# Kernel optimization log

Hardware: AMD Instinct MI355X
Metric: run time of the kernel (lower is better)

## Reference

```python
import jax, jax.numpy as jnp
import numpy as np

B, N_IN, NODE, L = 4, 128, 32, 256
N_HID, N_OUT = 64, 128
D_IN = N_HID          # d_inner = expand(1) * d_model
D_STATE = 2 * N_HID   # d_state = n_hid * 2
D_CONV = 2
DT_RANK = max(1, -(-N_HID // 16))  # ceil(d_model/16) = 4


def setup_inputs() -> dict:
    key = jax.random.key(0)
    ks = jax.random.split(key, 12)
    s = lambda k, shape, scale: (jax.random.normal(k, shape, jnp.float32) * scale)
    inputs = jax.random.normal(ks[0], (B, N_IN, NODE, L), jnp.float32)
    return {
        "inputs": inputs,
        "w_in": s(ks[1], (N_HID, N_IN), 1.0 / np.sqrt(N_IN)),
        "b_in": jnp.zeros((N_HID,), jnp.float32),
        "in_proj_w": s(ks[2], (2 * D_IN, N_HID), 1.0 / np.sqrt(N_HID)),
        "conv_w": s(ks[3], (D_IN, D_CONV), 0.5),
        "conv_b": jnp.zeros((D_IN,), jnp.float32),
        "x_proj_w": s(ks[4], (DT_RANK + 2 * D_STATE, D_IN), 1.0 / np.sqrt(D_IN)),
        "dt_proj_w": s(ks[5], (D_IN, DT_RANK), DT_RANK ** -0.5),
        "dt_proj_b": s(ks[6], (D_IN,), 0.1),
        "A_log": jnp.log(jnp.tile(jnp.arange(1, D_STATE + 1, dtype=jnp.float32)[None, :], (D_IN, 1))),
        "D": jnp.ones((D_IN,), jnp.float32),
        "out_proj_w": s(ks[7], (N_HID, D_IN), 1.0 / np.sqrt(D_IN)),
        "w_out": s(ks[8], (N_OUT, N_HID), 1.0 / np.sqrt(N_HID)),
        "b_out": jnp.zeros((N_OUT,), jnp.float32),
        "ln_w": jnp.ones((L, N_OUT), jnp.float32),
        "ln_b": jnp.zeros((L, N_OUT), jnp.float32),
    }


def _mamba(x, in_proj_w, conv_w, conv_b, x_proj_w, dt_proj_w, dt_proj_b, A_log, D, out_proj_w):
    # x: (Bseq, L, d_model)
    Bs, Ls, _ = x.shape
    d_state = A_log.shape[1]
    dt_rank = dt_proj_w.shape[1]
    d_conv = conv_w.shape[1]

    xz = x @ in_proj_w.T                     # (Bs, L, 2*d_inner)
    xm, z = jnp.split(xz, 2, axis=-1)

    # causal depthwise conv1d (padding = d_conv-1, truncated to L)
    xp = jnp.pad(xm, ((0, 0), (d_conv - 1, 0), (0, 0)))
    xc = sum(xp[:, k:k + Ls, :] * conv_w[:, k] for k in range(d_conv)) + conv_b
    xc = jax.nn.silu(xc)                     # (Bs, L, d_inner)

    dbc = xc @ x_proj_w.T                    # (Bs, L, dt_rank + 2*d_state)
    dt = dbc[..., :dt_rank]
    Bm = dbc[..., dt_rank:dt_rank + d_state]
    Cm = dbc[..., dt_rank + d_state:]
    delta = jax.nn.softplus(dt @ dt_proj_w.T + dt_proj_b)  # (Bs, L, d_inner)
    A = -jnp.exp(A_log)                      # (d_inner, d_state)

    def step(h, inp):
        dlt, Bt, Ct, xt = inp                # (Bs,d), (Bs,s), (Bs,s), (Bs,d)
        dA = jnp.exp(dlt[:, :, None] * A)    # (Bs, d, s)
        h = dA * h + (dlt * xt)[:, :, None] * Bt[:, None, :]
        y = jnp.einsum('bds,bs->bd', h, Ct)
        return h, y

    h0 = jnp.zeros((Bs, xm.shape[-1], d_state), x.dtype)
    xs = (delta.transpose(1, 0, 2), Bm.transpose(1, 0, 2),
          Cm.transpose(1, 0, 2), xc.transpose(1, 0, 2))
    _, ys = jax.lax.scan(step, h0, xs)       # ys: (L, Bs, d_inner)

    y = ys.transpose(1, 0, 2) + xc * D
    y = y * jax.nn.silu(z)
    return y @ out_proj_w.T                  # (Bs, L, d_model)


def reference(inputs, w_in, b_in, in_proj_w, conv_w, conv_b, x_proj_w,
              dt_proj_w, dt_proj_b, A_log, D, out_proj_w,
              w_out, b_out, ln_w, ln_b):
    b, n_in, node, seq = inputs.shape
    # permute(0,2,3,1).reshape(B*node, L, n_in)
    x = inputs.transpose(0, 2, 3, 1).reshape(b * node, seq, n_in)
    x = x @ w_in.T + b_in
    x = jax.nn.silu(_mamba(x, in_proj_w, conv_w, conv_b, x_proj_w,
                           dt_proj_w, dt_proj_b, A_log, D, out_proj_w))
    x = x @ w_out.T + b_out                  # (B*node, L, n_out)
    # LayerNorm over last two dims [feature_len, n_out]
    mu = x.mean(axis=(-2, -1), keepdims=True)
    var = ((x - mu) ** 2).mean(axis=(-2, -1), keepdims=True)
    x = (x - mu) / jnp.sqrt(var + 1e-5) * ln_w + ln_b
    return x.reshape(b, node, seq, -1).transpose(0, 3, 1, 2)
```

## Files before the change

### kernel.cpp

```cpp
#include <hip/hip_runtime.h>
#include <math.h>


__device__ __forceinline__ float silu_f(float v) { return v / (1.f + __expf(-v)); }
__device__ __forceinline__ float softplus_f(float v) { return v > 20.f ? v : log1pf(__expf(v)); }

__global__ __launch_bounds__(256) void k1_proj(
    const float* __restrict__ inp, const float* __restrict__ w_in,
    const float* __restrict__ b_in, const float* __restrict__ ipw,
    float* __restrict__ XM, float* __restrict__ Zb)
{
  __shared__ float sIN[128*64];
  __shared__ float sW[64*68];
  __shared__ float sXT[64*68];
  const int bid = blockIdx.x;
  const int r = bid >> 2, tb = bid & 3;
  const int b = r >> 5, node = r & 31;
  const int t0 = tb * 64;
  const int tid = threadIdx.x;
  const int tg = tid & 15, vg = tid >> 4;
  const int tl0 = tg * 4, v0 = vg * 4;

  for (int e = tid; e < 128*64; e += 256) {
    int i = e >> 6, t = e & 63;
    sIN[e] = inp[((b*128 + i)*32 + node)*256 + t0 + t];
  }

  float acc[4][4];
  #pragma unroll
  for (int ti = 0; ti < 4; ti++)
    #pragma unroll
    for (int j = 0; j < 4; j++) acc[ti][j] = b_in[v0 + j];

  for (int kc = 0; kc < 2; kc++) {
    __syncthreads();
    for (int e = tid; e < 64*16; e += 256) {
      int row = e >> 4, c4 = e & 15;
      *(float4*)&sW[row*68 + c4*4] = *(const float4*)&w_in[row*128 + kc*64 + c4*4];
    }
    __syncthreads();
    for (int k4 = 0; k4 < 16; k4++) {
      float4 wv[4];
      #pragma unroll
      for (int j = 0; j < 4; j++)
        wv[j] = *(const float4*)&sW[(v0 + j)*68 + k4*4];
      #pragma unroll
      for (int kk = 0; kk < 4; kk++) {
        float4 x4 = *(const float4*)&sIN[(kc*64 + k4*4 + kk)*64 + tl0];
        #pragma unroll
        for (int j = 0; j < 4; j++) {
          float w = kk==0 ? wv[j].x : kk==1 ? wv[j].y : kk==2 ? wv[j].z : wv[j].w;
          acc[0][j] = fmaf(x4.x, w, acc[0][j]);
          acc[1][j] = fmaf(x4.y, w, acc[1][j]);
          acc[2][j] = fmaf(x4.z, w, acc[2][j]);
          acc[3][j] = fmaf(x4.w, w, acc[3][j]);
        }
      }
    }
  }
  #pragma unroll
  for (int j = 0; j < 4; j++)
    *(float4*)&sXT[(v0 + j)*68 + tl0] =
        make_float4(acc[0][j], acc[1][j], acc[2][j], acc[3][j]);

  for (int pass = 0; pass < 2; pass++) {
    __syncthreads();
    for (int e = tid; e < 64*16; e += 256) {
      int row = e >> 4, c4 = e & 15;
      *(float4*)&sW[row*68 + c4*4] = *(const float4*)&ipw[(pass*64 + row)*64 + c4*4];
    }
    __syncthreads();

    float a2[4][4];
    #pragma unroll
    for (int ti = 0; ti < 4; ti++)
      #pragma unroll
      for (int j = 0; j < 4; j++) a2[ti][j] = 0.f;

    for (int k4 = 0; k4 < 16; k4++) {
      float4 wv[4];
      #pragma unroll
      for (int j = 0; j < 4; j++)
        wv[j] = *(const float4*)&sW[(v0 + j)*68 + k4*4];
      #pragma unroll
      for (int kk = 0; kk < 4; kk++) {
        float4 x4 = *(const float4*)&sXT[(k4*4 + kk)*68 + tl0];
        #pragma unroll
        for (int j = 0; j < 4; j++) {
          float w = kk==0 ? wv[j].x : kk==1 ? wv[j].y : kk==2 ? wv[j].z : wv[j].w;
          a2[0][j] = fmaf(x4.x, w, a2[0][j]);
          a2[1][j] = fmaf(x4.y, w, a2[1][j]);
          a2[2][j] = fmaf(x4.z, w, a2[2][j]);
          a2[3][j] = fmaf(x4.w, w, a2[3][j]);
        }
      }
    }

    float* dst = (pass == 0) ? XM : Zb;
    #pragma unroll
    for (int ti = 0; ti < 4; ti++)
      *(float4*)&dst[(r*256 + t0 + tl0 + ti)*64 + v0] =
          make_float4(a2[ti][0], a2[ti][1], a2[ti][2], a2[ti][3]);
  }
}

__global__ __launch_bounds__(256) void k2_conv_xproj(
    const float* __restrict__ XM, const float* __restrict__ convw,
    const float* __restrict__ convb, const float* __restrict__ xpw,
    const float* __restrict__ dtw, const float* __restrict__ dtb,
    float* __restrict__ XC, float* __restrict__ DELTA,
    float* __restrict__ BM, float* __restrict__ CM)
{
  __shared__ float sXM[65*64];
  __shared__ float sXC[64*68];
  __shared__ float sW[64*68];
  __shared__ float sDT[64*5];
  const int bid = blockIdx.x;
  const int r = bid >> 2, tb = bid & 3;
  const int t0 = tb * 64;
  const int tid = threadIdx.x;
  const int tg = tid & 15, vg = tid >> 4;
  const int tl0 = tg * 4, v0 = vg * 4;

  for (int e = tid; e < 65*64; e += 256) {
    int tt = e >> 6, d = e & 63;
    int tgl = t0 - 1 + tt;
    sXM[e] = (tgl < 0) ? 0.f : XM[(r*256 + tgl)*64 + d];
  }
  __syncthreads();

  for (int e = tid; e < 64*64; e += 256) {
    int t = e >> 6, d = e & 63;
    float c0 = convw[d*2], c1 = convw[d*2 + 1];
    float pre = fmaf(sXM[t*64 + d], c0, fmaf(sXM[(t+1)*64 + d], c1, convb[d]));
    float v = silu_f(pre);
    sXC[d*68 + t] = v;
    XC[(r*256 + t0 + t)*64 + d] = v;
  }

  for (int pass = 0; pass < 5; pass++) {
    __syncthreads();
    for (int e = tid; e < 64*16; e += 256) {
      int row = e >> 4, c4 = e & 15;
      int grow = pass*64 + row;
      float4 w = (grow < 260) ? *(const float4*)&xpw[grow*64 + c4*4]
                              : make_float4(0.f, 0.f, 0.f, 0.f);
      *(float4*)&sW[row*68 + c4*4] = w;
    }
    __syncthreads();

    float acc[4][4];
    #pragma unroll
    for (int ti = 0; ti < 4; ti++)
      #pragma unroll
      for (int jj = 0; jj < 4; jj++) acc[ti][jj] = 0.f;

    for (int k4 = 0; k4 < 16; k4++) {
      float4 wv[4];
      #pragma unroll
      for (int jj = 0; jj < 4; jj++)
        wv[jj] = *(const float4*)&sW[(v0 + jj)*68 + k4*4];
      #pragma unroll
      for (int kk = 0; kk < 4; kk++) {
        float4 x4 = *(const float4*)&sXC[(k4*4 + kk)*68 + tl0];
        #pragma unroll
        for (int jj = 0; jj < 4; jj++) {
          float w = kk==0 ? wv[jj].x : kk==1 ? wv[jj].y : kk==2 ? wv[jj].z : wv[jj].w;
          acc[0][jj] = fmaf(x4.x, w, acc[0][jj]);
          acc[1][jj] = fmaf(x4.y, w, acc[1][jj]);
          acc[2][jj] = fmaf(x4.z, w, acc[2][jj]);
          acc[3][jj] = fmaf(x4.w, w, acc[3][jj]);
        }
      }
    }

    const int j0g = pass*64 + v0;
    if (j0g < 4) {
      #pragma unroll
      for (int ti = 0; ti < 4; ti++)
        #pragma unroll
        for (int jj = 0; jj < 4; jj++)
          sDT[(tl0 + ti)*5 + jj] = acc[ti][jj];
    } else if (j0g < 132) {
      #pragma unroll
      for (int ti = 0; ti < 4; ti++)
        *(float4*)&BM[(r*256 + t0 + tl0 + ti)*128 + (j0g - 4)] =
            make_float4(acc[ti][0], acc[ti][1], acc[ti][2], acc[ti][3]);
    } else if (j0g < 260) {
      #pragma unroll
      for (int ti = 0; ti < 4; ti++)
        *(float4*)&CM[(r*256 + t0 + tl0 + ti)*128 + (j0g - 132)] =
            make_float4(acc[ti][0], acc[ti][1], acc[ti][2], acc[ti][3]);
    }
  }
  __syncthreads();

  for (int e = tid; e < 64*64; e += 256) {
    int t = e >> 6, d = e & 63;
    float4 w4 = *(const float4*)&dtw[d*4];
    float x = dtb[d];
    x = fmaf(sDT[t*5 + 0], w4.x, x);
    x = fmaf(sDT[t*5 + 1], w4.y, x);
    x = fmaf(sDT[t*5 + 2], w4.z, x);
    x = fmaf(sDT[t*5 + 3], w4.w, x);
    DELTA[(r*256 + t0 + t)*64 + d] = softplus_f(x);
  }
}

__global__ __launch_bounds__(256) void k3_scan(
    const float* __restrict__ DELTA, const float* __restrict__ XC,
    const float* __restrict__ BM, const float* __restrict__ CM,
    const float* __restrict__ alog, float* __restrict__ YP)
{
  __shared__ float sT[1280];
  const int bid = blockIdx.x;
  const int r = bid & 127;
  const int rest = bid >> 7;
  const int sc = rest & 1;
  const int dc = rest >> 1;
  const int tid = threadIdx.x;
  const int dg = tid >> 4;
  const int sg = tid & 15;
  const int sl0 = sg * 4;
  const int d = dc*16 + dg;
  const int sbase = sc*64 + sl0;

  float a[4], h[4];
  #pragma unroll
  for (int j = 0; j < 4; j++) {
    a[j] = -expf(alog[d*128 + sbase + j]);
    h[j] = 0.f;
  }

  const float* baseB = BM + r*256*128 + sc*64;
  const float* baseC = CM + r*256*128 + sc*64;
  const float* baseD = DELTA + r*256*64 + dc*16;
  const float* baseX = XC + r*256*64 + dc*16;

  float pre0, pre1, pre2, pre3, pre4;
  const int ttB = tid >> 6, qB = tid & 63;
  const int ttD = (tid & 127) >> 4, qD = tid & 15;

  #define K3_LOAD(tb_) do { \
    int t0_ = (tb_)*8; \
    pre0 = baseB[(t0_ + ttB)*128 + qB]; \
    pre1 = baseB[(t0_ + 4 + ttB)*128 + qB]; \
    pre2 = baseC[(t0_ + ttB)*128 + qB]; \
    pre3 = baseC[(t0_ + 4 + ttB)*128 + qB]; \
    pre4 = (tid < 128) ? baseD[(t0_ + ttD)*64 + qD] : baseX[(t0_ + ttD)*64 + qD]; \
  } while (0)

  #define K3_STORE() do { \
    sT[ttB*64 + qB] = pre0; \
    sT[(4 + ttB)*64 + qB] = pre1; \
    sT[512 + ttB*64 + qB] = pre2; \
    sT[512 + (4 + ttB)*64 + qB] = pre3; \
    sT[((tid < 128) ? 1024 : 1152) + ttD*16 + qD] = pre4; \
  } while (0)

  K3_LOAD(0);
  K3_STORE();
  __syncthreads();

  for (int tb = 0; tb < 32; tb++) {
    if (tb < 31) K3_LOAD(tb + 1);

    #pragma unroll
    for (int tt = 0; tt < 8; tt++) {
      float dl = sT[1024 + tt*16 + dg];
      float xv = sT[1152 + tt*16 + dg];
      float u  = dl * xv;
      float4 Bv = *(const float4*)&sT[tt*64 + sl0];
      float4 Cv = *(const float4*)&sT[512 + tt*64 + sl0];
      float y = 0.f;
      {
        float dA0 = __expf(dl * a[0]);
        h[0] = fmaf(dA0, h[0], u * Bv.x);
        y = fmaf(h[0], Cv.x, y);
        float dA1 = __expf(dl * a[1]);
        h[1] = fmaf(dA1, h[1], u * Bv.y);
        y = fmaf(h[1], Cv.y, y);
        float dA2 = __expf(dl * a[2]);
        h[2] = fmaf(dA2, h[2], u * Bv.z);
        y = fmaf(h[2], Cv.z, y);
        float dA3 = __expf(dl * a[3]);
        h[3] = fmaf(dA3, h[3], u * Bv.w);
        y = fmaf(h[3], Cv.w, y);
      }
      y += __shfl_xor(y, 1);
      y += __shfl_xor(y, 2);
      y += __shfl_xor(y, 4);
      y += __shfl_xor(y, 8);
      if (sg == 0)
        YP[((sc*128 + r)*256 + tb*8 + tt)*64 + d] = y;
    }

    __syncthreads();
    if (tb < 31) {
      K3_STORE();
      __syncthreads();
    }
  }
  #undef K3_LOAD
  #undef K3_STORE
}

__global__ __launch_bounds__(256) void k4_post(
    const float* __restrict__ YP, const float* __restrict__ XC,
    const float* __restrict__ Zb, const float* __restrict__ Dp,
    const float* __restrict__ opw, const float* __restrict__ wout,
    const float* __restrict__ bout, float* __restrict__ out,
    float* __restrict__ PSTAT)
{
  __shared__ float sY[64*68];
  __shared__ float sU[64*68];
  __shared__ float sW[64*68];
  __shared__ float sRs[256], sRq[256];
  const int bid = blockIdx.x;
  const int r = bid >> 2, tb = bid & 3;
  const int b = r >> 5, node = r & 31;
  const int t0 = tb * 64;
  const int tid = threadIdx.x;
  const int tg = tid & 15, vg = tid >> 4;
  const int tl0 = tg * 4, v0 = vg * 4;

  for (int e = tid; e < 64*64; e += 256) {
    int t = e >> 6, d = e & 63;
    int idx = (r*256 + t0 + t)*64 + d;
    float y = YP[idx] + YP[2097152 + idx];
    float y2 = fmaf(XC[idx], Dp[d], y);
    sY[d*68 + t] = y2 * silu_f(Zb[idx]);
  }

  __syncthreads();
  for (int e = tid; e < 64*16; e += 256) {
    int row = e >> 4, c4 = e & 15;
    *(float4*)&sW[row*68 + c4*4] = *(const float4*)&opw[row*64 + c4*4];
  }
  __syncthreads();

  {
    float acc[4][4];
    #pragma unroll
    for (int ti = 0; ti < 4; ti++)
      #pragma unroll
      for (int j = 0; j < 4; j++) acc[ti][j] = 0.f;
    for (int k4 = 0; k4 < 16; k4++) {
      float4 wv[4];
      #pragma unroll
      for (int j = 0; j < 4; j++)
        wv[j] = *(const float4*)&sW[(v0 + j)*68 + k4*4];
      #pragma unroll
      for (int kk = 0; kk < 4; kk++) {
        float4 x4 = *(const float4*)&sY[(k4*4 + kk)*68 + tl0];
        #pragma unroll
        for (int j = 0; j < 4; j++) {
          float w = kk==0 ? wv[j].x : kk==1 ? wv[j].y : kk==2 ? wv[j].z : wv[j].w;
          acc[0][j] = fmaf(x4.x, w, acc[0][j]);
          acc[1][j] = fmaf(x4.y, w, acc[1][j]);
          acc[2][j] = fmaf(x4.z, w, acc[2][j]);
          acc[3][j] = fmaf(x4.w, w, acc[3][j]);
        }
      }
    }
    #pragma unroll
    for (int j = 0; j < 4; j++)
      *(float4*)&sU[(v0 + j)*68 + tl0] =
          make_float4(silu_f(acc[0][j]), silu_f(acc[1][j]),
                      silu_f(acc[2][j]), silu_f(acc[3][j]));
  }

  float s = 0.f, q = 0.f;
  for (int pass = 0; pass < 2; pass++) {
    __syncthreads();
    for (int e = tid; e < 64*16; e += 256) {
      int row = e >> 4, c4 = e & 15;
      *(float4*)&sW[row*68 + c4*4] = *(const float4*)&wout[(pass*64 + row)*64 + c4*4];
    }
    __syncthreads();

    float a2[4][4];
    #pragma unroll
    for (int ti = 0; ti < 4; ti++)
      #pragma unroll
      for (int j = 0; j < 4; j++) a2[ti][j] = bout[pass*64 + v0 + j];

    for (int k4 = 0; k4 < 16; k4++) {
      float4 wv[4];
      #pragma unroll
      for (int j = 0; j < 4; j++)
        wv[j] = *(const float4*)&sW[(v0 + j)*68 + k4*4];
      #pragma unroll
      for (int kk = 0; kk < 4; kk++) {
        float4 x4 = *(const float4*)&sU[(k4*4 + kk)*68 + tl0];
        #pragma unroll
        for (int j = 0; j < 4; j++) {
          float w = kk==0 ? wv[j].x : kk==1 ? wv[j].y : kk==2 ? wv[j].z : wv[j].w;
          a2[0][j] = fmaf(x4.x, w, a2[0][j]);
          a2[1][j] = fmaf(x4.y, w, a2[1][j]);
          a2[2][j] = fmaf(x4.z, w, a2[2][j]);
          a2[3][j] = fmaf(x4.w, w, a2[3][j]);
        }
      }
    }

    #pragma unroll
    for (int ti = 0; ti < 4; ti++)
      #pragma unroll
      for (int j = 0; j < 4; j++) {
        float v = a2[ti][j];
        s += v;
        q = fmaf(v, v, q);
      }
    #pragma unroll
    for (int j = 0; j < 4; j++) {
      int o = pass*64 + v0 + j;
      *(float4*)&out[((b*128 + o)*32 + node)*256 + t0 + tl0] =
          make_float4(a2[0][j], a2[1][j], a2[2][j], a2[3][j]);
    }
  }

  sRs[tid] = s; sRq[tid] = q;
  __syncthreads();
  for (int st = 128; st > 0; st >>= 1) {
    if (tid < st) { sRs[tid] += sRs[tid + st]; sRq[tid] += sRq[tid + st]; }
    __syncthreads();
  }
  if (tid == 0) { PSTAT[bid*2] = sRs[0]; PSTAT[bid*2 + 1] = sRq[0]; }
}

__global__ __launch_bounds__(256) void k5_ln(
    const float* __restrict__ PSTAT, const float* __restrict__ lnw,
    const float* __restrict__ lnb, float* __restrict__ out)
{
  __shared__ float sLW[32*129], sLB[32*129];
  const int bid = blockIdx.x;
  const int r = bid >> 3, tb = bid & 7;
  const int b = r >> 5, node = r & 31;
  const int t0 = tb * 32;
  const int tid = threadIdx.x;

  float s = 0.f, q = 0.f;
  #pragma unroll
  for (int p = 0; p < 4; p++) {
    s += PSTAT[(r*4 + p)*2];
    q += PSTAT[(r*4 + p)*2 + 1];
  }
  const float mu = s * (1.f / 32768.f);
  const float var = q * (1.f / 32768.f) - mu * mu;
  const float rstd = rsqrtf(var + 1e-5f);

  for (int e = tid; e < 32*128; e += 256) {
    int t = e >> 7, o = e & 127;
    sLW[t*129 + o] = lnw[(t0 + t)*128 + o];
    sLB[t*129 + o] = lnb[(t0 + t)*128 + o];
  }
  __syncthreads();

  for (int n = 0; n < 16; n++) {
    int t = tid & 31;
    int o = (tid >> 5) + n*8;
    int idx = ((b*128 + o)*32 + node)*256 + t0 + t;
    float v = out[idx];
    out[idx] = fmaf((v - mu) * rstd, sLW[t*129 + o], sLB[t*129 + o]);
  }
}

extern "C" void kernel_launch(void* const* d_in, const int* in_sizes, int n_in,
                              void* d_out, int out_size, void* d_ws, size_t ws_size,
                              hipStream_t stream)
{
  (void)in_sizes; (void)n_in; (void)out_size; (void)ws_size;
  const float* inp   = (const float*)d_in[0];
  const float* w_in  = (const float*)d_in[1];
  const float* b_in  = (const float*)d_in[2];
  const float* ipw   = (const float*)d_in[3];
  const float* convw = (const float*)d_in[4];
  const float* convb = (const float*)d_in[5];
  const float* xpw   = (const float*)d_in[6];
  const float* dtw   = (const float*)d_in[7];
  const float* dtb   = (const float*)d_in[8];
  const float* alog  = (const float*)d_in[9];
  const float* Dp    = (const float*)d_in[10];
  const float* opw   = (const float*)d_in[11];
  const float* wout  = (const float*)d_in[12];
  const float* bout  = (const float*)d_in[13];
  const float* lnw   = (const float*)d_in[14];
  const float* lnb   = (const float*)d_in[15];

  float* ws = (float*)d_ws;
  float* XM    = ws + 0;
  float* Zb    = ws + 2097152;
  float* XC    = ws + 4194304;
  float* DELTA = ws + 6291456;
  float* BM    = ws + 8388608;
  float* CM    = ws + 12582912;
  float* YP    = ws + 16777216;
  float* PSTAT = ws + 20971520;
  float* out   = (float*)d_out;

  k1_proj<<<dim3(512), dim3(256), 0, stream>>>(inp, w_in, b_in, ipw, XM, Zb);
  k2_conv_xproj<<<dim3(512), dim3(256), 0, stream>>>(XM, convw, convb, xpw, dtw, dtb,
                                                     XC, DELTA, BM, CM);
  k3_scan<<<dim3(1024), dim3(256), 0, stream>>>(DELTA, XC, BM, CM, alog, YP);
  k4_post<<<dim3(512), dim3(256), 0, stream>>>(YP, XC, Zb, Dp, opw, wout, bout, out, PSTAT);
  k5_ln<<<dim3(1024), dim3(256), 0, stream>>>(PSTAT, lnw, lnb, out);
}
```

Before: 185.7 us.

## Double-buffer scan smem tiles with 16-step chunks and exp2 decay

The selective-scan kernel now uses two shared-memory buffers with 16 timesteps per chunk instead of one 8-step buffer. This halves the chunk count and cuts block barriers to one per chunk, with global prefetch running two chunks ahead. The decay exponent is prescaled by log2(e) so exp2f can be used directly, and the first y accumulate drops the zero add. In exchange it uses more LDS and registers per thread, which may lower occupancy.

Result: slower. 198.4 us (+6.8%).

```diff
diff --git a/kernel.cpp b/kernel.cpp
--- a/kernel.cpp
+++ b/kernel.cpp
@@ -212,7 +212,7 @@
     const float* __restrict__ BM, const float* __restrict__ CM,
     const float* __restrict__ alog, float* __restrict__ YP)
 {
-  __shared__ float sT[1280];
+  __shared__ float sT[2*2560];
   const int bid = blockIdx.x;
   const int r = bid & 127;
   const int rest = bid >> 7;
@@ -224,11 +224,12 @@
   const int sl0 = sg * 4;
   const int d = dc*16 + dg;
   const int sbase = sc*64 + sl0;
-
-  float a[4], h[4];
+  const float LOG2E = 1.44269504f;
+
+  float a2[4], h[4];
   #pragma unroll
   for (int j = 0; j < 4; j++) {
-    a[j] = -expf(alog[d*128 + sbase + j]);
+    a2[j] = -expf(alog[d*128 + sbase + j]) * LOG2E;
     h[j] = 0.f;
   }
 
@@ -237,53 +238,67 @@
   const float* baseD = DELTA + r*256*64 + dc*16;
   const float* baseX = XC + r*256*64 + dc*16;
 
-  float pre0, pre1, pre2, pre3, pre4;
-  const int ttB = tid >> 6, qB = tid & 63;
-  const int ttD = (tid & 127) >> 4, qD = tid & 15;
-
-  #define K3_LOAD(tb_) do { \
-    int t0_ = (tb_)*8; \
-    pre0 = baseB[(t0_ + ttB)*128 + qB]; \
-    pre1 = baseB[(t0_ + 4 + ttB)*128 + qB]; \
-    pre2 = baseC[(t0_ + ttB)*128 + qB]; \
-    pre3 = baseC[(t0_ + 4 + ttB)*128 + qB]; \
-    pre4 = (tid < 128) ? baseD[(t0_ + ttD)*64 + qD] : baseX[(t0_ + ttD)*64 + qD]; \
+  const int rowB = tid >> 6, colB = tid & 63;
+  const int rowD = tid >> 4, colD = tid & 15;
+  float pB[4], pC[4], pD, pX;
+
+  #define K3_LOADT(T_) do { \
+    int t0_ = (T_)*16; \
+    pB[0] = baseB[(t0_ + rowB     )*128 + colB]; \
+    pB[1] = baseB[(t0_ + rowB +  4)*128 + colB]; \
+    pB[2] = baseB[(t0_ + rowB +  8)*128 + colB]; \
+    pB[3] = baseB[(t0_ + rowB + 12)*128 + colB]; \
+    pC[0] = baseC[(t0_ + rowB     )*128 + colB]; \
+    pC[1] = baseC[(t0_ + rowB +  4)*128 + colB]; \
+    pC[2] = baseC[(t0_ + rowB +  8)*128 + colB]; \
+    pC[3] = baseC[(t0_ + rowB + 12)*128 + colB]; \
+    pD = baseD[(t0_ + rowD)*64 + colD]; \
+    pX = baseX[(t0_ + rowD)*64 + colD]; \
   } while (0)
 
-  #define K3_STORE() do { \
-    sT[ttB*64 + qB] = pre0; \
-    sT[(4 + ttB)*64 + qB] = pre1; \
-    sT[512 + ttB*64 + qB] = pre2; \
-    sT[512 + (4 + ttB)*64 + qB] = pre3; \
-    sT[((tid < 128) ? 1024 : 1152) + ttD*16 + qD] = pre4; \
+  #define K3_STORET(BUF_) do { \
+    float* S_ = &sT[(BUF_)*2560]; \
+    S_[(rowB     )*64 + colB] = pB[0]; \
+    S_[(rowB +  4)*64 + colB] = pB[1]; \
+    S_[(rowB +  8)*64 + colB] = pB[2]; \
+    S_[(rowB + 12)*64 + colB] = pB[3]; \
+    S_[1024 + (rowB     )*64 + colB] = pC[0]; \
+    S_[1024 + (rowB +  4)*64 + colB] = pC[1]; \
+    S_[1024 + (rowB +  8)*64 + colB] = pC[2]; \
+    S_[1024 + (rowB + 12)*64 + colB] = pC[3]; \
+    S_[2048 + rowD*16 + colD] = pD; \
+    S_[2304 + rowD*16 + colD] = pX; \
   } while (0)
 
-  K3_LOAD(0);
-  K3_STORE();
-  __syncthreads();
-
-  for (int tb = 0; tb < 32; tb++) {
-    if (tb < 31) K3_LOAD(tb + 1);
-
-    #pragma unroll
-    for (int tt = 0; tt < 8; tt++) {
-      float dl = sT[1024 + tt*16 + dg];
-      float xv = sT[1152 + tt*16 + dg];
+  K3_LOADT(0);
+  K3_STORET(0);
+  K3_LOADT(1);
+  __syncthreads();
+
+  for (int k = 0; k < 16; k++) {
+    if (k < 15) K3_STORET((k + 1) & 1);
+    if (k < 14) K3_LOADT(k + 2);
+
+    const float* S = &sT[(k & 1)*2560];
+    #pragma unroll
+    for (int tt = 0; tt < 16; tt++) {
+      float dl = S[2048 + tt*16 + dg];
+      float xv = S[2304 + tt*16 + dg];
       float u  = dl * xv;
-      float4 Bv = *(const float4*)&sT[tt*64 + sl0];
-      float4 Cv = *(const float4*)&sT[512 + tt*64 + sl0];
-      float y = 0.f;
+      float4 Bv = *(const float4*)&S[tt*64 + sl0];
+      float4 Cv = *(const float4*)&S[1024 + tt*64 + sl0];
+      float y;
       {
-        float dA0 = __expf(dl * a[0]);
+        float dA0 = exp2f(dl * a2[0]);
         h[0] = fmaf(dA0, h[0], u * Bv.x);
-        y = fmaf(h[0], Cv.x, y);
-        float dA1 = __expf(dl * a[1]);
+        y = h[0] * Cv.x;
+        float dA1 = exp2f(dl * a2[1]);
         h[1] = fmaf(dA1, h[1], u * Bv.y);
         y = fmaf(h[1], Cv.y, y);
-        float dA2 = __expf(dl * a[2]);
+        float dA2 = exp2f(dl * a2[2]);
         h[2] = fmaf(dA2, h[2], u * Bv.z);
         y = fmaf(h[2], Cv.z, y);
-        float dA3 = __expf(dl * a[3]);
+        float dA3 = exp2f(dl * a2[3]);
         h[3] = fmaf(dA3, h[3], u * Bv.w);
         y = fmaf(h[3], Cv.w, y);
       }
@@ -292,17 +307,13 @@
       y += __shfl_xor(y, 4);
       y += __shfl_xor(y, 8);
       if (sg == 0)
-        YP[((sc*128 + r)*256 + tb*8 + tt)*64 + d] = y;
-    }
-
-    __syncthreads();
-    if (tb < 31) {
-      K3_STORE();
-      __syncthreads();
-    }
-  }
-  #undef K3_LOAD
-  #undef K3_STORE
+        YP[((sc*128 + r)*256 + k*16 + tt)*64 + d] = y;
+    }
+
+    __syncthreads();
+  }
+  #undef K3_LOADT
+  #undef K3_STORET
 }
 
 __global__ __launch_bounds__(256) void k4_post(
```
